# Kernel optimization log

Measured on AMD Instinct MI355X. Metric: run time of the kernel, lower is better.

Reference implementation:

```python
import jax, jax.numpy as jnp
import numpy as np

ALPHA = 0.2
BETA = 1.0
TEMPERATURE = 0.05
EPS = 1e-8  # torch cosine_similarity eps


def setup_inputs() -> dict:
    key = jax.random.key(0)
    k1, k2 = jax.random.split(key)
    B, R, D = 4096, 18, 256  # rows, segment size (1 anchor + 1 pos + 16 negs), embed dim
    features = jax.random.normal(k1, (B * R, D), dtype=jnp.float32)
    scores = jax.random.normal(k2, (B * (R - 1),), dtype=jnp.float32)
    row_sizes = jnp.full((B,), R, dtype=jnp.int32)  # uniform ragged sizes
    logit_scale = jnp.array([1.0 / TEMPERATURE], dtype=jnp.float32)
    return {"features": features, "scores": scores, "row_sizes": row_sizes,
            "logit_scale": logit_scale}


def reference(features, scores, row_sizes, logit_scale):
    B = row_sizes.shape[0]
    R = features.shape[0] // B  # uniform segment size
    D = features.shape[1]
    f3 = features.reshape(B, R, D)
    anchor = f3[:, 0]          # [B, D]
    tgt = f3[:, 1:]            # [B, R-1, D]  (positive first, then negatives)

    # --- per-row cosine sims + log_softmax + KLDiv(batchmean) ---
    an = jnp.maximum(jnp.linalg.norm(anchor, axis=-1, keepdims=True), EPS)  # [B,1]
    tn = jnp.maximum(jnp.linalg.norm(tgt, axis=-1), EPS)                    # [B,R-1]
    cos = jnp.einsum('bd,bkd->bk', anchor, tgt) / (an * tn)                 # [B,R-1]
    emb_log = jax.nn.log_softmax(cos, axis=-1)                              # [B,R-1]
    ce = jax.nn.softmax(scores.reshape(B, R - 1), axis=-1)                  # [B,R-1]
    # torch KLDivLoss(reduction='batchmean') on a length-(R-1) vector divides by (R-1)
    kl = jnp.sum(ce * (jnp.log(ce) - emb_log), axis=-1) / (R - 1)           # [B]
    loss = jnp.mean(BETA * kl)

    # --- single InfoNCE over all rows: anchors vs [positives; all negatives] ---
    pos = f3[:, 1]                                   # [B, D]
    negs = f3[:, 2:].reshape(B * (R - 2), D)         # [B*(R-2), D]
    targets = jnp.concatenate([pos, negs], axis=0)   # [B*(R-1), D]
    logits = logit_scale[0] * (anchor @ targets.T)   # [B, B*(R-1)]
    labels = jnp.arange(B)
    # cross_entropy(logits, labels) with mean reduction
    infonce = jnp.mean(jax.nn.logsumexp(logits, axis=-1) - logits[labels, labels])

    return loss + ALPHA * infonce
```

## Files before the change

kernel.cpp:

```cpp
#include <hip/hip_runtime.h>
#include <math.h>

#define ALPHA 0.2f
#define BETA 1.0f
#define EPSV 1e-8f
#define LOG2E 1.4426950408889634f
#define LN2 0.6931471805599453f

#define BATCH 4096
#define RR 18
#define KT 17
#define DD 256
#define NTGT (BATCH*KT)
#define NTILE (NTGT/32)
#define TILE_BYTES (32*DD)

#define AG 64
#define NSPLIT 64
#define TPS (NTILE/NSPLIT)

#define EXPA 8388608.0f
#define EXPB 1064880320.0f

typedef int   i32x8  __attribute__((ext_vector_type(8)));
typedef float f32x16 __attribute__((ext_vector_type(16)));

__device__ inline int pk8(float a, float b, float c, float d){
  int p = __builtin_amdgcn_cvt_pk_fp8_f32(a, b, 0, false);
  return  __builtin_amdgcn_cvt_pk_fp8_f32(c, d, p, true);
}

__device__ inline float fmax3(float a, float b, float c){
  return fmaxf(fmaxf(a, b), c);
}

__device__ inline float fexp2u(float x, float kc){
  float t = fmaf(x, EXPA, kc);
  unsigned u;
  asm("v_cvt_u32_f32 %0, %1" : "=v"(u) : "v"(t));
  return __uint_as_float(u);
}


__global__ __launch_bounds__(256) void prep_kernel(
    const float* __restrict__ feat, const float* __restrict__ scores,
    const float* __restrict__ lscale,
    unsigned char* __restrict__ abf8, unsigned char* __restrict__ tbf8,
    float* __restrict__ diag, float* __restrict__ klarr,
    float* __restrict__ out){
  __shared__ float csh[KT];
  __shared__ uint4 fsh[16][KT];
  int b = blockIdx.x, tid = threadIdx.x;
  int grp = tid >> 4, j = tid & 15;
  const float* fb = feat + (size_t)b * RR * DD;
  float s2 = lscale[0] * LOG2E;

  if (b == 0 && tid == 0) out[0] = 0.f;

  float4 a0 = ((const float4*)fb)[j*4+0];
  float4 a1 = ((const float4*)fb)[j*4+1];
  float4 a2 = ((const float4*)fb)[j*4+2];
  float4 a3 = ((const float4*)fb)[j*4+3];
  float asq = (a0.x*a0.x+a0.y*a0.y+a0.z*a0.z+a0.w*a0.w)
            + (a1.x*a1.x+a1.y*a1.y+a1.z*a1.z+a1.w*a1.w)
            + (a2.x*a2.x+a2.y*a2.y+a2.z*a2.z+a2.w*a2.w)
            + (a3.x*a3.x+a3.y*a3.y+a3.z*a3.z+a3.w*a3.w);
  #pragma unroll
  for (int off=1; off<16; off<<=1) asq += __shfl_xor(asq, off);
  float an = fmaxf(sqrtf(asq), EPSV);

  if (tid < 16){
    uint4 v = make_uint4(
      (unsigned)pk8(a0.x*s2,a0.y*s2,a0.z*s2,a0.w*s2),
      (unsigned)pk8(a1.x*s2,a1.y*s2,a1.z*s2,a1.w*s2),
      (unsigned)pk8(a2.x*s2,a2.y*s2,a2.z*s2,a2.w*s2),
      (unsigned)pk8(a3.x*s2,a3.y*s2,a3.z*s2,a3.w*s2));
    *(uint4*)(abf8 + (size_t)b*DD + j*16) = v;
  }

  for (int kr = grp+1; kr <= KT; kr += 16){
    const float4* tp = (const float4*)(fb + (size_t)kr*DD) + j*4;
    float4 t0=tp[0], t1=tp[1], t2=tp[2], t3=tp[3];
    uint4 v = make_uint4(
      (unsigned)pk8(t0.x,t0.y,t0.z,t0.w), (unsigned)pk8(t1.x,t1.y,t1.z,t1.w),
      (unsigned)pk8(t2.x,t2.y,t2.z,t2.w), (unsigned)pk8(t3.x,t3.y,t3.z,t3.w));
    fsh[j][kr-1] = v;
    float d = (a0.x*t0.x+a0.y*t0.y+a0.z*t0.z+a0.w*t0.w)
            + (a1.x*t1.x+a1.y*t1.y+a1.z*t1.z+a1.w*t1.w)
            + (a2.x*t2.x+a2.y*t2.y+a2.z*t2.z+a2.w*t2.w)
            + (a3.x*t3.x+a3.y*t3.y+a3.z*t3.z+a3.w*t3.w);
    float q = (t0.x*t0.x+t0.y*t0.y+t0.z*t0.z+t0.w*t0.w)
            + (t1.x*t1.x+t1.y*t1.y+t1.z*t1.z+t1.w*t1.w)
            + (t2.x*t2.x+t2.y*t2.y+t2.z*t2.z+t2.w*t2.w)
            + (t3.x*t3.x+t3.y*t3.y+t3.z*t3.z+t3.w*t3.w);
    #pragma unroll
    for (int off=1; off<16; off<<=1){ d += __shfl_xor(d,off); q += __shfl_xor(q,off); }
    if (j == 0){
      csh[kr-1] = d / (an * fmaxf(sqrtf(q), EPSV));
      if (kr == 1) diag[b] = d;
    }
  }
  __syncthreads();

  for (int idx = tid; idx < 16*KT; idx += 256){
    int jj = idx / KT, r = idx % KT;
    uint4 v = fsh[jj][r];
    int t = b*KT + r;
    int tile = t >> 5, m = t & 31;
    int ki = jj >> 2, hf = (jj >> 1) & 1, w = jj & 1;
    *(uint4*)(tbf8 + (size_t)tile*TILE_BYTES + ki*2048 + w*1024 + hf*512 + m*16) = v;
  }

  if (tid < 64){
    bool act = tid < KT;
    float c  = act ? csh[tid] : -INFINITY;
    float sv = act ? scores[(size_t)b*KT + tid] : -INFINITY;
    float cm = c, sm = sv;
    #pragma unroll
    for (int off=1; off<64; off<<=1){
      cm = fmaxf(cm, __shfl_xor(cm, off));
      sm = fmaxf(sm, __shfl_xor(sm, off));
    }
    float ec = act ? __builtin_amdgcn_exp2f((c -cm)*LOG2E) : 0.f;
    float es = act ? __builtin_amdgcn_exp2f((sv-sm)*LOG2E) : 0.f;
    float cs = ec, ss = es;
    #pragma unroll
    for (int off=1; off<64; off<<=1){
      cs += __shfl_xor(cs, off);
      ss += __shfl_xor(ss, off);
    }
    float lse_c = cm + __logf(cs);
    float lse_s = sm + __logf(ss);
    float kt = 0.f;
    if (act){
      float lq = sv - lse_s;
      float lp = c  - lse_c;
      kt = __builtin_amdgcn_exp2f(lq*LOG2E)*(lq - lp);
    }
    #pragma unroll
    for (int off=1; off<64; off<<=1) kt += __shfl_xor(kt, off);
    if (tid == 0) klarr[b] = kt * (1.0f/KT);
  }
}

__global__ __launch_bounds__(64,2) void gemm_lse_kernel(
    const unsigned char* __restrict__ abf8, const unsigned char* __restrict__ tbf8,
    float* __restrict__ part_m, float* __restrict__ part_s){
  const int bid  = blockIdx.x;
  const int ns   = (bid & 7)*8 + ((bid >> 3) & 7);
  const int ag   = bid >> 6;
  const int lane = threadIdx.x;
  const int l31  = lane & 31;
  const int half = lane >> 5;

  i32x8 af[2][4];
  {
    const unsigned char* ab = abf8 + (size_t)ag*64*DD;
    #pragma unroll
    for (int nt=0;nt<2;++nt)
      #pragma unroll
      for (int ki=0;ki<4;++ki){
        const unsigned char* p = ab + (size_t)(nt*32+l31)*DD + ki*64 + half*32;
        uint4* h = (uint4*)&af[nt][ki];
        h[0] = *(const uint4*)p;
        h[1] = *(const uint4*)(p+16);
      }
  }

  const unsigned char* gbase =
      tbf8 + (size_t)(ns*TPS)*TILE_BYTES + half*512 + l31*16;

  i32x8 ta[4], tb[4];
  auto ld = [&](int tt, i32x8 tf[4]){
    const unsigned char* p = gbase + (size_t)tt*TILE_BYTES;
    #pragma unroll
    for (int ki=0;ki<4;++ki){
      uint4* h = (uint4*)&tf[ki];
      h[0] = *(const uint4*)(p + ki*2048);
      h[1] = *(const uint4*)(p + ki*2048 + 1024);
    }
  };

  float run_m[2] = {-INFINITY,-INFINITY};
  float run_s[2] = {0.f,0.f};
  f32x16 acc[2];
  const f32x16 vzero = (f32x16)(0.f);

  auto mfma_tile = [&](i32x8 tf[4]){
    __builtin_amdgcn_s_setprio(1);
    acc[0] = __builtin_amdgcn_mfma_scale_f32_32x32x64_f8f6f4(
                 tf[0], af[0][0], vzero, 0,0, 0,127, 0,127);
    acc[1] = __builtin_amdgcn_mfma_scale_f32_32x32x64_f8f6f4(
                 tf[0], af[1][0], vzero, 0,0, 0,127, 0,127);
    #pragma unroll
    for (int ki=1;ki<4;++ki){
      acc[0] = __builtin_amdgcn_mfma_scale_f32_32x32x64_f8f6f4(
                   tf[ki], af[0][ki], acc[0], 0,0, 0,127, 0,127);
      acc[1] = __builtin_amdgcn_mfma_scale_f32_32x32x64_f8f6f4(
                   tf[ki], af[1][ki], acc[1], 0,0, 0,127, 0,127);
    }
    __builtin_amdgcn_s_setprio(0);
  };

  auto epilogue = [&](){
    #pragma unroll
    for (int nt=0;nt<2;++nt){
      f32x16 t = acc[nt];
      float x0 = fmax3(t[0], t[1], t[2]);
      float x1 = fmax3(t[3], t[4], t[5]);
      float x2 = fmax3(t[6], t[7], t[8]);
      float x3 = fmax3(t[9], t[10], t[11]);
      float x4 = fmax3(t[12], t[13], t[14]);
      float mx = fmaxf(fmax3(x0,x1,x2), fmax3(x3,x4,t[15]));

      float kc = fmaf(mx, -EXPA, EXPB);
      float s0=0.f, s1=0.f, s2=0.f, s3=0.f;
      #pragma unroll
      for (int r=0;r<16;r+=4){
        s0 += fexp2u(t[r  ],kc);
        s1 += fexp2u(t[r+1],kc);
        s2 += fexp2u(t[r+2],kc);
        s3 += fexp2u(t[r+3],kc);
      }
      float sh = (s0+s1)+(s2+s3);

      float nm = fmaxf(run_m[nt], mx);
      run_s[nt] = run_s[nt]*__builtin_amdgcn_exp2f(run_m[nt]-nm)
                + sh*__builtin_amdgcn_exp2f(mx-nm);
      run_m[nt] = nm;
    }
  };

  ld(0, ta);
  ld(1, tb);
  for (int t=0; t<TPS; t+=2){
    mfma_tile(ta);
    if (t+2 < TPS) ld(t+2, ta);
    epilogue();
    mfma_tile(tb);
    if (t+3 < TPS) ld(t+3, tb);
    epilogue();
  }

  #pragma unroll
  for (int nt=0;nt<2;++nt){
    float om = __shfl_xor(run_m[nt], 32);
    float os = __shfl_xor(run_s[nt], 32);
    float nm = fmaxf(run_m[nt], om);
    float S  = run_s[nt]*__builtin_amdgcn_exp2f(run_m[nt]-nm)
             + os*__builtin_amdgcn_exp2f(om-nm);
    if (half == 0){
      int gm = ag*64 + nt*32 + l31;
      part_m[(size_t)ns*BATCH + gm] = nm;
      part_s[(size_t)ns*BATCH + gm] = S;
    }
  }
}

__global__ __launch_bounds__(256) void combine_kernel(
    const float* __restrict__ part_m, const float* __restrict__ part_s,
    const float* __restrict__ diag, const float* __restrict__ klarr,
    const float* __restrict__ lscale, float* __restrict__ out){
  int tid = threadIdx.x;
  int b = blockIdx.x*256 + tid;
  float s = lscale[0];
  float m = -INFINITY, S = 0.f;
  #pragma unroll
  for (int ns=0; ns<NSPLIT; ++ns){
    float pm_ = part_m[(size_t)ns*BATCH + b];
    float ps_ = part_s[(size_t)ns*BATCH + b];
    float nm = fmaxf(m, pm_);
    S = S*__builtin_amdgcn_exp2f(m-nm) + ps_*__builtin_amdgcn_exp2f(pm_-nm);
    m = nm;
  }
  float inf = (m + __log2f(S))*LN2 - s*diag[b];
  float c = BETA*klarr[b] + ALPHA*inf;
  #pragma unroll
  for (int off=1; off<64; off<<=1) c += __shfl_xor(c, off);
  if ((tid & 63) == 0) atomicAdd(out, c*(1.0f/BATCH));
}

extern "C" void kernel_launch(void* const* d_in, const int* in_sizes, int n_in,
                              void* d_out, int out_size, void* d_ws, size_t ws_size,
                              hipStream_t stream){
  const float* feat   = (const float*)d_in[0];
  const float* scores = (const float*)d_in[1];
  const float* lscale = (const float*)d_in[3];

  float* ws     = (float*)d_ws;
  float* diag   = ws;
  float* klarr  = diag + BATCH;
  float* part_m = klarr + BATCH;
  float* part_s = part_m + (size_t)NSPLIT*BATCH;
  unsigned char* abf8 = (unsigned char*)(part_s + (size_t)NSPLIT*BATCH);
  unsigned char* tbf8 = abf8 + (size_t)BATCH*DD;

  float* outp = (float*)d_out;
  prep_kernel<<<BATCH, 256, 0, stream>>>(feat, scores, lscale, abf8, tbf8,
                                         diag, klarr, outp);
  gemm_lse_kernel<<<AG*NSPLIT, 64, 0, stream>>>(abf8, tbf8, part_m, part_s);
  combine_kernel<<<BATCH/256, 256, 0, stream>>>(part_m, part_s, diag, klarr,
                                                lscale, outp);
}
```

Measured before the change: 194.8 us.

## Stage target tiles through LDS with async global_load_lds double buffering

Target tiles are now loaded straight from global memory into a double-buffered LDS area using global_load_lds, then read into registers per tile. The old path loaded them from global memory directly into registers. Explicit vmcnt/lgkmcnt waits order the pipeline. NSPLIT is halved, so each block handles twice as many tiles and the grid is half the size. The aim is to free VGPRs and hide load latency, but the change adds LDS traffic and reduces parallelism.

```diff
diff --git a/kernel.cpp b/kernel.cpp
--- a/kernel.cpp
+++ b/kernel.cpp
@@ -16,7 +16,7 @@
 #define TILE_BYTES (32*DD)
 
 #define AG 64
-#define NSPLIT 64
+#define NSPLIT 32
 #define TPS (NTILE/NSPLIT)
 
 #define EXPA 8388608.0f
@@ -24,6 +24,12 @@
 
 typedef int   i32x8  __attribute__((ext_vector_type(8)));
 typedef float f32x16 __attribute__((ext_vector_type(16)));
+
+__device__ inline void gl_lds16(const void* g, void* l){
+  __builtin_amdgcn_global_load_lds(
+      (const __attribute__((address_space(1))) unsigned int*)g,
+      (__attribute__((address_space(3))) unsigned int*)l, 16, 0, 0);
+}
 
 __device__ inline int pk8(float a, float b, float c, float d){
   int p = __builtin_amdgcn_cvt_pk_fp8_f32(a, b, 0, false);
@@ -146,9 +152,10 @@
 __global__ __launch_bounds__(64,2) void gemm_lse_kernel(
     const unsigned char* __restrict__ abf8, const unsigned char* __restrict__ tbf8,
     float* __restrict__ part_m, float* __restrict__ part_s){
+  __shared__ __align__(16) unsigned char Bs[2][TILE_BYTES];
   const int bid  = blockIdx.x;
-  const int ns   = (bid & 7)*8 + ((bid >> 3) & 7);
-  const int ag   = bid >> 6;
+  const int ns   = (bid & 7)*4 + ((bid >> 3) & 3);
+  const int ag   = bid >> 5;
   const int lane = threadIdx.x;
   const int l31  = lane & 31;
   const int half = lane >> 5;
@@ -167,20 +174,15 @@
       }
   }
 
-  const unsigned char* gbase =
-      tbf8 + (size_t)(ns*TPS)*TILE_BYTES + half*512 + l31*16;
-
-  i32x8 ta[4], tb[4];
-  auto ld = [&](int tt, i32x8 tf[4]){
-    const unsigned char* p = gbase + (size_t)tt*TILE_BYTES;
-    #pragma unroll
-    for (int ki=0;ki<4;++ki){
-      uint4* h = (uint4*)&tf[ki];
-      h[0] = *(const uint4*)(p + ki*2048);
-      h[1] = *(const uint4*)(p + ki*2048 + 1024);
-    }
-  };
-
+  const unsigned char* gt = tbf8 + (size_t)(ns*TPS)*TILE_BYTES + lane*16;
+  auto stage = [&](int t, int b){
+    const unsigned char* g = gt + (size_t)t*TILE_BYTES;
+    #pragma unroll
+    for (int j=0;j<8;++j)
+      gl_lds16(g + j*1024, &Bs[b][j*1024 + lane*16]);
+  };
+
+  const int lbase = half*512 + l31*16;
   float run_m[2] = {-INFINITY,-INFINITY};
   float run_s[2] = {0.f,0.f};
   f32x16 acc[2];
@@ -231,14 +233,41 @@
     }
   };
 
-  ld(0, ta);
-  ld(1, tb);
-  for (int t=0; t<TPS; t+=2){
-    mfma_tile(ta);
-    if (t+2 < TPS) ld(t+2, ta);
+  auto tfread0 = [&](i32x8 tf[4]){
+    #pragma unroll
+    for (int ki=0;ki<4;++ki){
+      uint4* h = (uint4*)&tf[ki];
+      h[0] = *(const uint4*)(&Bs[0][lbase + ki*2048]);
+      h[1] = *(const uint4*)(&Bs[0][lbase + ki*2048 + 1024]);
+    }
+  };
+  auto tfread1 = [&](i32x8 tf[4]){
+    #pragma unroll
+    for (int ki=0;ki<4;++ki){
+      uint4* h = (uint4*)&tf[ki];
+      h[0] = *(const uint4*)(&Bs[1][lbase + ki*2048]);
+      h[1] = *(const uint4*)(&Bs[1][lbase + ki*2048 + 1024]);
+    }
+  };
+
+  stage(0, 0);
+  stage(1, 1);
+
+  for (int t = 0; t < TPS; t += 2){
+    if (t+1 < TPS) asm volatile("s_waitcnt vmcnt(8)" ::: "memory");
+    else           asm volatile("s_waitcnt vmcnt(0)" ::: "memory");
+    i32x8 tf[4];
+    tfread0(tf);
+    asm volatile("s_waitcnt lgkmcnt(0)" ::: "memory");
+    if (t+2 < TPS) stage(t+2, 0);
+    mfma_tile(tf);
     epilogue();
-    mfma_tile(tb);
-    if (t+3 < TPS) ld(t+3, tb);
+    if (t+2 < TPS) asm volatile("s_waitcnt vmcnt(8)" ::: "memory");
+    else           asm volatile("s_waitcnt vmcnt(0)" ::: "memory");
+    tfread1(tf);
+    asm volatile("s_waitcnt lgkmcnt(0)" ::: "memory");
+    if (t+3 < TPS) stage(t+3, 1);
+    mfma_tile(tf);
     epilogue();
   }
 
```

Measured after the change: 190.2 us. 2.4% less time.
